# Performance work log

Measured on AMD Instinct MI355X. Metric: run time of the kernel, lower is better.

Reference implementation:

```python
import jax, jax.numpy as jnp
import numpy as np
from jax import lax

B_BLK = 16   # block size B
N_Z = 64     # latent dim


def setup_inputs() -> dict:
    key = jax.random.key(0)
    ks = jax.random.split(key, 6)
    in_ch, out_ch = 256, 256
    L = (out_ch // B_BLK) * (in_ch // B_BLK)  # 256 latent codes
    x = jax.random.normal(ks[0], (32, in_ch, 64, 64), dtype=jnp.float32)
    z = jax.random.normal(ks[1], (L, N_Z), dtype=jnp.float32)
    W1 = jax.random.normal(ks[2], (B_BLK, N_Z, N_Z), dtype=jnp.float32) * 0.1
    B1 = jax.random.normal(ks[3], (B_BLK, N_Z), dtype=jnp.float32) * 0.1
    W2 = jax.random.normal(ks[4], (B_BLK, B_BLK * 9, N_Z), dtype=jnp.float32) * 0.1
    B2 = jax.random.normal(ks[5], (B_BLK, B_BLK * 9), dtype=jnp.float32) * 0.1
    return {"x": x, "z": z, "W1": W1, "B1": B1, "W2": W2, "B2": B2}


def _aggregate_weight(z, W1, B1, W2, B2, out_ch, in_ch):
    # hypertype='separate', batched over all L = (out_ch//B)*(in_ch//B) blocks.
    # per block: a = W1 @ z + B1 -> (B, N_z); K = W2 @ a[...,None] + B2 -> (B, B*9)
    a = jnp.einsum('bdn,ln->lbd', W1, z) + B1            # (L, B, N_z)
    K = jnp.einsum('bkd,lbd->lbk', W2, a) + B2           # (L, B, B*9)
    ob, ib = out_ch // B_BLK, in_ch // B_BLK
    K = K.reshape(ob, ib, B_BLK, B_BLK, 3, 3)            # (o_blk, i_blk, b1, b2, 3, 3)
    # torch: K.reshape(B,B,3,3).permute(1,0,2,3) => weight_block[p,q] = K[q,p]
    # then cat over i_blk on dim 1 (in), over o_blk on dim 0 (out)
    w = K.transpose(0, 3, 1, 2, 4, 5)                    # (o_blk, b2, i_blk, b1, 3, 3)
    return w.reshape(out_ch, in_ch, 3, 3)


def reference(x, z, W1, B1, W2, B2):
    out_ch, in_ch = 256, 256
    weight = _aggregate_weight(z, W1, B1, W2, B2, out_ch, in_ch)
    # F.conv2d(x, weight, bias=None, stride=1, padding=kernel_size//2=1)
    return lax.conv_general_dilated(
        x, weight,
        window_strides=(1, 1),
        padding=[(1, 1), (1, 1)],
        dimension_numbers=('NCHW', 'OIHW', 'NCHW'))
```

## Files before the change

kernel.cpp:

```cpp
#include <hip/hip_runtime.h>

typedef unsigned short u16;
typedef unsigned int u32;
typedef __attribute__((ext_vector_type(8))) short short8;
typedef __attribute__((ext_vector_type(4))) float f32x4;
typedef __attribute__((ext_vector_type(4))) unsigned short u16x4;

__device__ __forceinline__ u16 f2bf(float f) {
    u32 u = __float_as_uint(f);
    return (u16)((u + 0x7FFFu + ((u >> 16) & 1u)) >> 16);
}

__device__ __forceinline__ void gl2lds16(const u16* g, u16* l) {
    __builtin_amdgcn_global_load_lds(
        (const __attribute__((address_space(1))) u32*)g,
        (__attribute__((address_space(3))) u32*)l, 16, 0, 0);
}

__global__ __launch_bounds__(256) void nchw2nhwc(const float* __restrict__ x,
                                                 u16* __restrict__ xb) {
    __shared__ u16 t[64 * 72];
    const int b   = blockIdx.x;
    const int n   = b >> 8;
    const int icb = (b >> 6) & 3;
    const int pxb = b & 63;
    const int ic0 = icb * 64, px0 = pxb * 64;
    const int tid = threadIdx.x;

    const int icq = tid >> 4;
    const int px4 = (tid & 15) * 4;
    const float* src = x + (size_t)(n * 256 + ic0 + icq * 4) * 4096 + px0 + px4;
    f32x4 v[4];
#pragma unroll
    for (int rr = 0; rr < 4; ++rr) v[rr] = *(const f32x4*)(src + (size_t)rr * 4096);
#pragma unroll
    for (int j = 0; j < 4; ++j) {
        u16x4 p;
        p.x = f2bf(v[0][j]); p.y = f2bf(v[1][j]);
        p.z = f2bf(v[2][j]); p.w = f2bf(v[3][j]);
        *(u16x4*)(t + (px4 + j) * 72 + icq * 4) = p;
    }
    __syncthreads();

    const int c = tid & 7, pxr = tid >> 3;
    u16* dstb = xb + ((size_t)(n * 4096) + px0) * 256 + ic0 + c * 8;
#pragma unroll
    for (int h = 0; h < 2; ++h) {
        int px = h * 32 + pxr;
        uint4 val = *(const uint4*)(t + px * 72 + c * 8);
        *(uint4*)(dstb + (size_t)px * 256) = val;
    }
}

__global__ __launch_bounds__(256) void wgen(const float* __restrict__ z,
                                            const float* __restrict__ W1,
                                            const float* __restrict__ B1,
                                            const float* __restrict__ W2,
                                            const float* __restrict__ B2,
                                            u16* __restrict__ wb,
                                            u16* __restrict__ zpad) {
    __shared__ float zl[64];
    __shared__ float aL[1024];
    const int l = blockIdx.x;
    const int tid = threadIdx.x;
    if (l == 0 && tid < 32) zpad[tid] = 0;
    if (tid < 64) zl[tid] = z[l * 64 + tid];
    __syncthreads();
#pragma unroll
    for (int i = 0; i < 4; ++i) {
        int idx = i * 256 + tid;
        const float* wrow = W1 + (size_t)idx * 64;
        float s = B1[idx];
        for (int nn = 0; nn < 64; ++nn) s += wrow[nn] * zl[nn];
        aL[idx] = s;
    }
    __syncthreads();
    const int b1 = tid >> 4, b2 = tid & 15;
    const int ob = l >> 4, ib = l & 15;
    const int ic = ib * 16 + b1;
    const int oc = ob * 16 + b2;
    const size_t wbase = (size_t)oc * 2304 + (size_t)(ic >> 5) * 288 + (ic & 31);
    const float* arow = aL + b1 * 64;
#pragma unroll
    for (int tap = 0; tap < 9; ++tap) {
        int kk = b2 * 9 + tap;
        const float* w2row = W2 + (size_t)(b1 * 144 + kk) * 64;
        float s = B2[b1 * 144 + kk];
        for (int d = 0; d < 64; ++d) s += w2row[d] * arow[d];
        wb[wbase + tap * 32] = f2bf(s);
    }
}

__global__ __launch_bounds__(256) void conv_mfma(const u16* __restrict__ xb,
                                                 const u16* __restrict__ wb,
                                                 const u16* __restrict__ zpad,
                                                 float* __restrict__ out) {
    __shared__ __align__(16) u16 As[128 * 32];
    __shared__ __align__(16) u16 Bs[128 * 32];

    const int tid = threadIdx.x;
    const int bid = blockIdx.x;
    const int xcd = bid & 7, rest = bid >> 3;
    const int mt = rest & 1, grp = rest >> 1;
    const int nt = grp * 8 + xcd;
    const int n = nt >> 5;
    const int pimg = (nt & 31) << 7;
    const int oc0 = mt << 7;

    const int lane = tid & 63;
    const int wave = tid >> 6;
    const int wm = (wave >> 1) & 1, wn = wave & 1;
    const int lr = lane & 15, lq = lane >> 4;

    const int r0 = tid >> 2, c0 = tid & 3;
    const int q1 = tid + 256, r1 = q1 >> 2, c1 = q1 & 3;

    const u16* aw0 = wb + (size_t)(oc0 + r0) * 2304 + c0 * 8;
    const u16* aw1 = wb + (size_t)(oc0 + r1) * 2304 + c1 * 8;
    u16* al0 = As + tid * 8;
    u16* al1 = As + (tid + 256) * 8;
    u16* bl0 = Bs + tid * 8;
    u16* bl1 = Bs + (tid + 256) * 8;

    const int po0 = pimg + r0, po1 = pimg + r1;
    const int ho0 = po0 >> 6, wo0 = po0 & 63;
    const int ho1 = po1 >> 6, wo1 = po1 & 63;
    const u16* bx0 = xb + ((size_t)(n * 4096) + po0) * 256 + c0 * 8;
    const u16* bx1 = xb + ((size_t)(n * 4096) + po1) * 256 + c1 * 8;

    bool m0[9], m1[9];
#pragma unroll
    for (int tap = 0; tap < 9; ++tap) {
        const int dh = tap / 3 - 1, dw = tap % 3 - 1;
        m0[tap] = ((unsigned)(ho0 + dh) < 64u) & ((unsigned)(wo0 + dw) < 64u);
        m1[tap] = ((unsigned)(ho1 + dh) < 64u) & ((unsigned)(wo1 + dw) < 64u);
    }

    f32x4 acc[4][4];
    const f32x4 z4 = {0.f, 0.f, 0.f, 0.f};
#pragma unroll
    for (int i = 0; i < 4; ++i)
#pragma unroll
        for (int j = 0; j < 4; ++j) acc[i][j] = z4;

    for (int icb = 0; icb < 8; ++icb) {
#pragma unroll
        for (int tap = 0; tap < 9; ++tap) {
            const int dh = tap / 3 - 1, dw = tap % 3 - 1;
            const int toff = (dh * 64 + dw) * 256 + icb * 32;
            const int koff = (icb * 9 + tap) * 32;

            gl2lds16(aw0 + koff, al0);
            gl2lds16(aw1 + koff, al1);
            gl2lds16(m0[tap] ? bx0 + toff : zpad, bl0);
            gl2lds16(m1[tap] ? bx1 + toff : zpad, bl1);
            __syncthreads();

            short8 af[4], bfr[4];
#pragma unroll
            for (int i = 0; i < 4; ++i) {
                af[i]  = *(const short8*)(As + (wm * 64 + i * 16 + lr) * 32 + lq * 8);
                bfr[i] = *(const short8*)(Bs + (wn * 64 + i * 16 + lr) * 32 + lq * 8);
            }
#pragma unroll
            for (int i = 0; i < 4; ++i)
#pragma unroll
                for (int j = 0; j < 4; ++j)
                    acc[i][j] = __builtin_amdgcn_mfma_f32_16x16x32_bf16(
                        af[i], bfr[j], acc[i][j], 0, 0, 0);
            __syncthreads();
        }
    }

    const size_t outn = (size_t)n * 256 * 4096;
#pragma unroll
    for (int i = 0; i < 4; ++i) {
        int ocb = oc0 + wm * 64 + i * 16 + lq * 4;
#pragma unroll
        for (int j = 0; j < 4; ++j) {
            int po = pimg + wn * 64 + j * 16 + lr;
            float* op = out + outn + (size_t)ocb * 4096 + po;
#pragma unroll
            for (int r = 0; r < 4; ++r) op[(size_t)r * 4096] = acc[i][j][r];
        }
    }
}

extern "C" void kernel_launch(void* const* d_in, const int* in_sizes, int n_in,
                              void* d_out, int out_size, void* d_ws, size_t ws_size,
                              hipStream_t stream) {
    const float* x  = (const float*)d_in[0];
    const float* z  = (const float*)d_in[1];
    const float* W1 = (const float*)d_in[2];
    const float* B1 = (const float*)d_in[3];
    const float* W2 = (const float*)d_in[4];
    const float* B2 = (const float*)d_in[5];
    float* out = (float*)d_out;

    u16* xb = (u16*)d_ws;
    u16* wb = xb + (size_t)32 * 4096 * 256;
    u16* zp = wb + (size_t)256 * 2304;
    const size_t need = ((size_t)32 * 4096 * 256 + (size_t)256 * 2304 + 32) * 2;
    if (ws_size < need) return;

    nchw2nhwc<<<dim3(8192), dim3(256), 0, stream>>>(x, xb);
    wgen<<<dim3(256), dim3(256), 0, stream>>>(z, W1, B1, W2, B2, wb, zp);
    conv_mfma<<<dim3(2048), dim3(256), 0, stream>>>(xb, wb, zp, out);
}
```

Baseline: 469.3 us.

## Reuse halo input rows across horizontal taps and prefetch through registers in conv

The conv kernel now stages one input row with a halo (66 pixels per output row) plus weights for all three horizontal taps in LDS per step. That cuts the K loop from 72 to 24 staged steps, with three MFMA sweeps per stage reading shifted B rows. Global loads of the next stage go into registers while the current stage computes, replacing the direct global-to-LDS copies and the zero-pad buffer. The weight layout is reorganised to [icb,kh][oc][kw,ic], and wgen is rewritten with vectorised coalesced loads and shuffle reductions. The cost is more LDS, extra register pressure from the prefetch buffers, and padded strides that may still cause bank conflicts.

After: 928.0 us. 97.7% more time.

```diff
diff --git a/kernel.cpp b/kernel.cpp
--- a/kernel.cpp
+++ b/kernel.cpp
@@ -9,12 +9,6 @@
 __device__ __forceinline__ u16 f2bf(float f) {
     u32 u = __float_as_uint(f);
     return (u16)((u + 0x7FFFu + ((u >> 16) & 1u)) >> 16);
-}
-
-__device__ __forceinline__ void gl2lds16(const u16* g, u16* l) {
-    __builtin_amdgcn_global_load_lds(
-        (const __attribute__((address_space(1))) u32*)g,
-        (__attribute__((address_space(3))) u32*)l, 16, 0, 0);
 }
 
 __global__ __launch_bounds__(256) void nchw2nhwc(const float* __restrict__ x,
@@ -57,83 +51,80 @@
                                             const float* __restrict__ B1,
                                             const float* __restrict__ W2,
                                             const float* __restrict__ B2,
-                                            u16* __restrict__ wb,
-                                            u16* __restrict__ zpad) {
+                                            u16* __restrict__ wb) {
     __shared__ float zl[64];
     __shared__ float aL[1024];
-    const int l = blockIdx.x;
-    const int tid = threadIdx.x;
-    if (l == 0 && tid < 32) zpad[tid] = 0;
+    const int l = blockIdx.x, tid = threadIdx.x;
     if (tid < 64) zl[tid] = z[l * 64 + tid];
     __syncthreads();
-#pragma unroll
-    for (int i = 0; i < 4; ++i) {
-        int idx = i * 256 + tid;
-        const float* wrow = W1 + (size_t)idx * 64;
-        float s = B1[idx];
-        for (int nn = 0; nn < 64; ++nn) s += wrow[nn] * zl[nn];
-        aL[idx] = s;
+    const int g = tid >> 4, c = tid & 15;
+    const f32x4 zc = *(const f32x4*)(zl + c * 4);
+    for (int it = 0; it < 64; ++it) {
+        int r = it * 16 + g;
+        f32x4 w = *(const f32x4*)(W1 + (size_t)r * 64 + c * 4);
+        float p = w.x * zc.x + w.y * zc.y + w.z * zc.z + w.w * zc.w;
+        if (c == 0) p += B1[r];
+        p += __shfl_xor(p, 1); p += __shfl_xor(p, 2);
+        p += __shfl_xor(p, 4); p += __shfl_xor(p, 8);
+        if (c == 0) aL[r] = p;
     }
     __syncthreads();
-    const int b1 = tid >> 4, b2 = tid & 15;
     const int ob = l >> 4, ib = l & 15;
-    const int ic = ib * 16 + b1;
-    const int oc = ob * 16 + b2;
-    const size_t wbase = (size_t)oc * 2304 + (size_t)(ic >> 5) * 288 + (ic & 31);
-    const float* arow = aL + b1 * 64;
-#pragma unroll
-    for (int tap = 0; tap < 9; ++tap) {
-        int kk = b2 * 9 + tap;
-        const float* w2row = W2 + (size_t)(b1 * 144 + kk) * 64;
-        float s = B2[b1 * 144 + kk];
-        for (int d = 0; d < 64; ++d) s += w2row[d] * arow[d];
-        wb[wbase + tap * 32] = f2bf(s);
+    for (int b1 = 0; b1 < 16; ++b1) {
+        const f32x4 ac = *(const f32x4*)(aL + b1 * 64 + c * 4);
+        const int ic = ib * 16 + b1;
+#pragma unroll
+        for (int it = 0; it < 9; ++it) {
+            int kk = it * 16 + g;
+            f32x4 w = *(const f32x4*)(W2 + (size_t)(b1 * 144 + kk) * 64 + c * 4);
+            float p = w.x * ac.x + w.y * ac.y + w.z * ac.z + w.w * ac.w;
+            if (c == 0) p += B2[b1 * 144 + kk];
+            p += __shfl_xor(p, 1); p += __shfl_xor(p, 2);
+            p += __shfl_xor(p, 4); p += __shfl_xor(p, 8);
+            if (c == 0) {
+                int b2 = kk / 9, tap = kk % 9;
+                int oc = ob * 16 + b2;
+                int s = (ic >> 5) * 3 + tap / 3;
+                wb[(size_t)s * 24576 + oc * 96 + (tap % 3) * 32 + (ic & 31)] = f2bf(p);
+            }
+        }
     }
 }
 
 __global__ __launch_bounds__(256) void conv_mfma(const u16* __restrict__ xb,
                                                  const u16* __restrict__ wb,
-                                                 const u16* __restrict__ zpad,
                                                  float* __restrict__ out) {
-    __shared__ __align__(16) u16 As[128 * 32];
-    __shared__ __align__(16) u16 Bs[128 * 32];
-
-    const int tid = threadIdx.x;
-    const int bid = blockIdx.x;
+    __shared__ __align__(16) u16 As[128 * 104];
+    __shared__ __align__(16) u16 Bs[132 * 40];
+
+    const int tid = threadIdx.x, bid = blockIdx.x;
     const int xcd = bid & 7, rest = bid >> 3;
     const int mt = rest & 1, grp = rest >> 1;
     const int nt = grp * 8 + xcd;
     const int n = nt >> 5;
-    const int pimg = (nt & 31) << 7;
+    const int h0 = (nt & 31) * 2;
+    const int pimg = h0 * 64;
     const int oc0 = mt << 7;
 
-    const int lane = tid & 63;
-    const int wave = tid >> 6;
-    const int wm = (wave >> 1) & 1, wn = wave & 1;
+    const int lane = tid & 63, wave = tid >> 6;
+    const int wm = wave >> 1, wn = wave & 1;
     const int lr = lane & 15, lq = lane >> 4;
 
-    const int r0 = tid >> 2, c0 = tid & 3;
-    const int q1 = tid + 256, r1 = q1 >> 2, c1 = q1 & 3;
-
-    const u16* aw0 = wb + (size_t)(oc0 + r0) * 2304 + c0 * 8;
-    const u16* aw1 = wb + (size_t)(oc0 + r1) * 2304 + c1 * 8;
-    u16* al0 = As + tid * 8;
-    u16* al1 = As + (tid + 256) * 8;
-    u16* bl0 = Bs + tid * 8;
-    u16* bl1 = Bs + (tid + 256) * 8;
-
-    const int po0 = pimg + r0, po1 = pimg + r1;
-    const int ho0 = po0 >> 6, wo0 = po0 & 63;
-    const int ho1 = po1 >> 6, wo1 = po1 & 63;
-    const u16* bx0 = xb + ((size_t)(n * 4096) + po0) * 256 + c0 * 8;
-    const u16* bx1 = xb + ((size_t)(n * 4096) + po1) * 256 + c1 * 8;
-
-    bool m0[9], m1[9];
-#pragma unroll
-    for (int tap = 0; tap < 9; ++tap) {
-        const int dh = tap / 3 - 1, dw = tap % 3 - 1;
-        m0[tap] = ((unsigned)(ho0 + dh) < 64u) & ((unsigned)(wo0 + dw) < 64u);
-        m1[tap] = ((unsigned)(ho1 + dh) < 64u) & ((unsigned)(wo1 + dw) < 64u);
+    const int arow = tid >> 1, ahalf = tid & 1;
+    const u16* aptr = wb + (size_t)(oc0 + arow) * 96 + ahalf * 48;
+    u16* alds = As + arow * 104 + ahalf * 48;
+
+    int hrw[3], ldso[3]; bool vw[3]; long gbase[3];
+#pragma unroll
+    for (int k = 0; k < 3; ++k) {
+        int q = (k == 0) ? tid : (k == 1) ? tid + 256 : 512 + tid;
+        int prow = q >> 2, icc = q & 3;
+        int hr = prow >= 66 ? 1 : 0;
+        int w = prow - hr * 66 - 1;
+        hrw[k] = hr;
+        vw[k] = (unsigned)w < 64u;
+        gbase[k] = ((long)n * 4096 + w) * 256 + icc * 8;
+        ldso[k] = prow * 40 + icc * 8;
     }
 
     f32x4 acc[4][4];
@@ -143,33 +134,59 @@
 #pragma unroll
         for (int j = 0; j < 4; ++j) acc[i][j] = z4;
 
-    for (int icb = 0; icb < 8; ++icb) {
-#pragma unroll
-        for (int tap = 0; tap < 9; ++tap) {
-            const int dh = tap / 3 - 1, dw = tap % 3 - 1;
-            const int toff = (dh * 64 + dw) * 256 + icb * 32;
-            const int koff = (icb * 9 + tap) * 32;
-
-            gl2lds16(aw0 + koff, al0);
-            gl2lds16(aw1 + koff, al1);
-            gl2lds16(m0[tap] ? bx0 + toff : zpad, bl0);
-            gl2lds16(m1[tap] ? bx1 + toff : zpad, bl1);
-            __syncthreads();
-
-            short8 af[4], bfr[4];
-#pragma unroll
-            for (int i = 0; i < 4; ++i) {
-                af[i]  = *(const short8*)(As + (wm * 64 + i * 16 + lr) * 32 + lq * 8);
-                bfr[i] = *(const short8*)(Bs + (wn * 64 + i * 16 + lr) * 32 + lq * 8);
+    uint4 pa[6], pb[3];
+    const uint4 zz = {0u, 0u, 0u, 0u};
+
+#pragma unroll
+    for (int cc = 0; cc < 6; ++cc) pa[cc] = *(const uint4*)(aptr + cc * 8);
+#pragma unroll
+    for (int k = 0; k < 3; ++k) {
+        int h = h0 + hrw[k] - 1;
+        bool v = vw[k] && ((unsigned)h < 64u);
+        pb[k] = v ? *(const uint4*)(xb + gbase[k] + (long)h * 16384) : zz;
+    }
+
+    int icb = 0, kh = 0;
+    for (int s = 0; s < 24; ++s) {
+#pragma unroll
+        for (int cc = 0; cc < 6; ++cc) *(uint4*)(alds + cc * 8) = pa[cc];
+        *(uint4*)(Bs + ldso[0]) = pb[0];
+        *(uint4*)(Bs + ldso[1]) = pb[1];
+        if (tid < 16) *(uint4*)(Bs + ldso[2]) = pb[2];
+        __syncthreads();
+
+        int nkh = kh + 1, nicb = icb;
+        if (nkh == 3) { nkh = 0; ++nicb; }
+        if (s < 23) {
+            const u16* ap = aptr + (size_t)(s + 1) * 24576;
+#pragma unroll
+            for (int cc = 0; cc < 6; ++cc) pa[cc] = *(const uint4*)(ap + cc * 8);
+#pragma unroll
+            for (int k = 0; k < 3; ++k) {
+                int h = h0 + hrw[k] - 1 + nkh;
+                bool v = vw[k] && ((unsigned)h < 64u);
+                pb[k] = v ? *(const uint4*)(xb + gbase[k] + (long)h * 16384 + nicb * 32) : zz;
             }
+        }
+
+#pragma unroll
+        for (int dwo = 0; dwo < 3; ++dwo) {
+            short8 af[4], bf[4];
+#pragma unroll
+            for (int i = 0; i < 4; ++i)
+                af[i] = *(const short8*)(As + (wm * 64 + i * 16 + lr) * 104 + dwo * 32 + lq * 8);
+#pragma unroll
+            for (int j = 0; j < 4; ++j)
+                bf[j] = *(const short8*)(Bs + (wn * 66 + j * 16 + lr + dwo) * 40 + lq * 8);
 #pragma unroll
             for (int i = 0; i < 4; ++i)
 #pragma unroll
                 for (int j = 0; j < 4; ++j)
                     acc[i][j] = __builtin_amdgcn_mfma_f32_16x16x32_bf16(
-                        af[i], bfr[j], acc[i][j], 0, 0, 0);
-            __syncthreads();
-        }
+                        af[i], bf[j], acc[i][j], 0, 0, 0);
+        }
+        __syncthreads();
+        icb = nicb; kh = nkh;
     }
 
     const size_t outn = (size_t)n * 256 * 4096;
@@ -199,11 +216,10 @@
 
     u16* xb = (u16*)d_ws;
     u16* wb = xb + (size_t)32 * 4096 * 256;
-    u16* zp = wb + (size_t)256 * 2304;
-    const size_t need = ((size_t)32 * 4096 * 256 + (size_t)256 * 2304 + 32) * 2;
+    const size_t need = ((size_t)32 * 4096 * 256 + (size_t)24 * 256 * 96) * 2;
     if (ws_size < need) return;
 
     nchw2nhwc<<<dim3(8192), dim3(256), 0, stream>>>(x, xb);
-    wgen<<<dim3(256), dim3(256), 0, stream>>>(z, W1, B1, W2, B2, wb, zp);
-    conv_mfma<<<dim3(2048), dim3(256), 0, stream>>>(xb, wb, zp, out);
-}
+    wgen<<<dim3(256), dim3(256), 0, stream>>>(z, W1, B1, W2, B2, wb);
+    conv_mfma<<<dim3(2048), dim3(256), 0, stream>>>(xb, wb, out);
+}
```
